# Kernel tuning notes

Measured on AMD Instinct MI355X. Metric: run time of the kernel, lower is better.

Reference implementation:

```python
import jax, jax.numpy as jnp
import numpy as np

TOPK = 3
IOU_THRESHOLD = 0.5


def setup_inputs() -> dict:
    key = jax.random.key(0)
    k0, k1, k2, k3 = jax.random.split(key, 4)
    S, N, TGT_PER_VID = 256, 128, 4
    M = S * TGT_PER_VID          # 1024 target moments total
    P = N * N                    # 16384 valid proposals (mask2d all ones)
    start_offset = jax.random.normal(k0, (S, P), dtype=jnp.float32) * 0.1
    end_offset = jax.random.normal(k1, (S, P), dtype=jnp.float32) * 0.1
    # target moments: (start, end) in [0,1], start <= end
    tgt_moments = jnp.sort(jax.random.uniform(k2, (M, 2), dtype=jnp.float32), axis=1)
    num_targets = jnp.full((S,), TGT_PER_VID, dtype=jnp.int32)  # sums to M
    iou2ds = jax.random.uniform(k3, (M, N, N), dtype=jnp.float32)
    mask2d = jnp.ones((N, N), dtype=bool)
    return {
        "start_offset": start_offset,
        "end_offset": end_offset,
        "tgt_moments": tgt_moments,
        "num_targets": num_targets,
        "iou2ds": iou2ds,
        "mask2d": mask2d,
    }


def reference(start_offset, end_offset, tgt_moments, num_targets, iou2ds, mask2d):
    M, N, _ = iou2ds.shape
    S, P = start_offset.shape
    # map each of the M targets back to its source video (repeat_interleave)
    scatter_m2s = jnp.repeat(jnp.arange(S), num_targets, total_repeat_length=M)
    so = start_offset[scatter_m2s]  # [M, P]
    eo = end_offset[scatter_m2s]    # [M, P]
    # row-major nonzero positions of mask2d (== torch masked_select ordering)
    rows, cols = jnp.nonzero(mask2d, size=P)
    iou1ds = iou2ds[:, rows, cols]  # [M, P]
    # top-k scatter mask + IoU-threshold mask
    _, topk_idx = jax.lax.top_k(iou1ds, TOPK)  # [M, TOPK]
    target_mask = jnp.zeros((M, P), dtype=start_offset.dtype)
    target_mask = target_mask.at[jnp.arange(M)[:, None], topk_idx].set(1.0)
    target_mask = jnp.where(iou1ds > IOU_THRESHOLD, 1.0, target_mask)
    # scores2ds_to_moments: proposal (row, col) -> moment (row/N, (col+1)/N)
    starts = rows.astype(start_offset.dtype) / N                 # [P]
    ends = (cols.astype(start_offset.dtype) + 1.0) / N           # [P]
    start_offset_target = tgt_moments[:, 0:1] - starts[None, :]  # [M, P]
    end_offset_target = tgt_moments[:, 1:2] - ends[None, :]      # [M, P]
    loss = jnp.abs(so - start_offset_target) + jnp.abs(eo - end_offset_target)
    return (loss * target_mask).sum() / target_mask.sum()
```

## Files before the change

kernel.cpp:

```cpp
#include <hip/hip_runtime.h>
#include <math.h>

#define IOU_THR 0.5f
#define NCNT 8
#define FS 8
#define GS 2
#define TPV 4
#define SENT 0x7fffffff

__device__ __forceinline__ bool better(float va, int ia, float vb, int ib) {
    return (va > vb) || (va == vb && ia < ib);
}

__device__ __forceinline__ void merge3(float& a0, float& a1, float& a2,
                                       int& x0, int& x1, int& x2,
                                       float b0, float b1, float b2,
                                       int y0, int y1, int y2) {
    bool t0 = better(a0, x0, b0, y0);
    float ov0 = t0 ? a0 : b0;  int oi0 = t0 ? x0 : y0;
    float ahv = t0 ? a1 : a0;  int ahi = t0 ? x1 : x0;
    float a2v = t0 ? a2 : a1;  int a2i = t0 ? x2 : x1;
    float bhv = t0 ? b0 : b1;  int bhi = t0 ? y0 : y1;
    float b2v = t0 ? b1 : b2;  int b2i = t0 ? y1 : y2;
    bool t1 = better(ahv, ahi, bhv, bhi);
    float ov1 = t1 ? ahv : bhv; int oi1 = t1 ? ahi : bhi;
    float cav = t1 ? a2v : ahv; int cai = t1 ? a2i : ahi;
    float cbv = t1 ? bhv : b2v; int cbi = t1 ? bhi : b2i;
    bool t2 = better(cav, cai, cbv, cbi);
    a0 = ov0; a1 = ov1; a2 = t2 ? cav : cbv;
    x0 = oi0; x1 = oi1; x2 = t2 ? cai : cbi;
}

__global__ void prep_kernel(const int* __restrict__ num_targets,
                            const int* __restrict__ mask2d,
                            int* __restrict__ scatter,
                            int* __restrict__ counts,
                            int* __restrict__ uniform_flag,
                            int S, int M, int P) {
    const int bid = blockIdx.x;
    const int tid = threadIdx.x;

    if (bid < NCNT) {
        const int P4 = P >> 2;
        const int4* __restrict__ m4 = (const int4*)mask2d;
        int c = 0;
        for (int q = bid * 256 + tid; q < P4; q += NCNT * 256) {
            const int4 v = m4[q];
            c += (v.x != 0) + (v.y != 0) + (v.z != 0) + (v.w != 0);
        }
        if (bid == 0) {
            for (int j = (P4 << 2) + tid; j < P; j += 256)
                c += (mask2d[j] != 0);
        }
        __shared__ int red[256];
        red[tid] = c;
        __syncthreads();
        for (int st = 128; st > 0; st >>= 1) {
            if (tid < st) red[tid] += red[tid + st];
            __syncthreads();
        }
        if (tid == 0) counts[bid] = red[0];
    } else {
        __shared__ int cum[1025];
        __shared__ int scn[256];
        __shared__ int uni[256];
        const int chunk = (S + 255) / 256;
        const int sbase = tid * chunk;
        int local[4];
        int csum = 0;
        int ok = 1;
        for (int k = 0; k < chunk && k < 4; ++k) {
            int s = sbase + k;
            int v = (s < S) ? num_targets[s] : TPV;
            if (s < S && v != TPV) ok = 0;
            csum += (s < S) ? v : 0;
            local[k] = csum;
        }
        scn[tid] = csum;
        uni[tid] = ok;
        __syncthreads();
        for (int d = 1; d < 256; d <<= 1) {
            int v = scn[tid];
            int add = (tid >= d) ? scn[tid - d] : 0;
            __syncthreads();
            scn[tid] = v + add;
            __syncthreads();
        }
        for (int st = 128; st > 0; st >>= 1) {
            if (tid < st) uni[tid] &= uni[tid + st];
            __syncthreads();
        }
        {
            int excl = scn[tid] - csum;
            for (int k = 0; k < chunk && k < 4; ++k) {
                int s = sbase + k;
                if (s < S) cum[s + 1] = excl + local[k];
            }
            if (tid == 0) cum[0] = 0;
        }
        __syncthreads();
        const int total = cum[S];
        if (tid == 0)
            uniform_flag[0] = (uni[0] && total == M && M == TPV * S) ? 1 : 0;
        for (int m = tid; m < M; m += 256) {
            int mm = m;
            if (mm >= total) mm = (total > 0) ? (total - 1) : 0;
            int lo = 0, hi = S - 1;
            while (lo < hi) {
                int mid = (lo + hi) >> 1;
                if (cum[mid + 1] <= mm) lo = mid + 1; else hi = mid;
            }
            scatter[m] = lo;
        }
    }
}

__global__ void build_kernel(const int* __restrict__ counts,
                             const int* __restrict__ mask2d,
                             int* __restrict__ rcidx,
                             float* __restrict__ starts,
                             float* __restrict__ ends,
                             int* __restrict__ flag,
                             int N, int P) {
    const int tid = threadIdx.x;
    __shared__ int scan[256];

    scan[tid] = (tid < NCNT) ? counts[tid] : 0;
    __syncthreads();
    for (int st = 128; st > 0; st >>= 1) {
        if (tid < st) scan[tid] += scan[tid + st];
        __syncthreads();
    }
    const int K_all = scan[0];
    const int f = (K_all == P && (P & 3) == 0 && (N & (N - 1)) == 0 && N >= 4) ? 1 : 0;
    if (tid == 0) flag[0] = f;
    if (f) return;
    __syncthreads();

    const int per = (P + 255) / 256;
    const int base = tid * per;
    int cnt = 0;
    for (int k = 0; k < per; ++k) {
        int j = base + k;
        if (j < P && mask2d[j] != 0) cnt++;
    }
    scan[tid] = cnt;
    __syncthreads();
    for (int d = 1; d < 256; d <<= 1) {
        int v = scan[tid];
        int add = (tid >= d) ? scan[tid - d] : 0;
        __syncthreads();
        scan[tid] = v + add;
        __syncthreads();
    }
    const int K = scan[255];
    int pos = scan[tid] - cnt;

    const float fN = (float)N;
    for (int k = 0; k < per; ++k) {
        int j = base + k;
        if (j < P && mask2d[j] != 0) {
            int r = j / N;
            int c = j - r * N;
            rcidx[pos]  = j;
            starts[pos] = (float)r / fN;
            ends[pos]   = (float)(c + 1) / fN;
            pos++;
        }
    }
    __syncthreads();
    for (int j = K + tid; j < P; j += 256) {
        rcidx[j]  = 0;
        starts[j] = 0.0f;
        ends[j]   = 1.0f / fN;
    }
}

__global__ __launch_bounds__(256, 4)
void loss_kernel(const float* __restrict__ start_offset,
                 const float* __restrict__ end_offset,
                 const float* __restrict__ tgt_moments,
                 const int* __restrict__ scatter,
                 const float* __restrict__ iou2ds,
                 const int* __restrict__ rcidx,
                 const float* __restrict__ starts,
                 const float* __restrict__ ends,
                 float* __restrict__ opv, int* __restrict__ opi,
                 double* __restrict__ ops, int* __restrict__ opc,
                 const int* __restrict__ flag,
                 const int* __restrict__ uflag,
                 int P, int M, int N) {
    const int blk = blockIdx.x;
    const int tid = threadIdx.x;
    const int fp  = flag[0];
    const int P4  = P >> 2;
    const bool grouped = fp && uflag[0] && ((M & 1) == 0) &&
                         (P4 % (GS * 256 * 4) == 0);
    const int   lgN  = 31 - __clz(N);
    const float invN = 1.0f / (float)N;

#define PROC(ST, v, jj, so_, eo_, A_, B_)                                   \
    do {                                                                    \
        const bool b0 = (v) > v0##ST;                                       \
        const bool b1 = (v) > v1##ST;                                       \
        const bool b2 = (v) > v2##ST;                                       \
        const float nv0 = fmaxf(v0##ST, (v));                               \
        const float nv1 = __builtin_amdgcn_fmed3f((v), v0##ST, v1##ST);     \
        const float nv2 = __builtin_amdgcn_fmed3f((v), v1##ST, v2##ST);     \
        i2##ST = b1 ? i1##ST : (b2 ? (jj) : i2##ST);                        \
        i1##ST = b0 ? i0##ST : (b1 ? (jj) : i1##ST);                        \
        i0##ST = b0 ? (jj) : i0##ST;                                        \
        v0##ST = nv0; v1##ST = nv1; v2##ST = nv2;                           \
        const bool sel = (v) > IOU_THR;                                     \
        const float l_ = fabsf((so_) - (A_)) + fabsf((eo_) - (B_));         \
        ls##ST += sel ? l_ : 0.0f;                                          \
        lc##ST += sel ? 1 : 0;                                              \
    } while (0)

    if (grouped) {
        if (blk >= M) return;
        int m0, half;
        const int HM = M >> 1;
        if ((HM & 7) == 0 && (M & 3) == 0) {
            const int g = blk % HM, dup = blk / HM;
            m0 = ((g >> 1) << 2) + (dup << 1);
            half = g & 1;
        } else {
            m0 = blk & ~1;
            half = blk & 1;
        }
        const int m1 = m0 + 1;
        const int s  = scatter[m0];

        const float4* __restrict__ so4 = (const float4*)(start_offset + (size_t)s * P);
        const float4* __restrict__ eo4 = (const float4*)(end_offset   + (size_t)s * P);
        const float4* __restrict__ ioA = (const float4*)(iou2ds + (size_t)m0 * P);
        const float4* __restrict__ ioB = (const float4*)(iou2ds + (size_t)m1 * P);
        const float t00 = tgt_moments[2 * m0],     t10 = tgt_moments[2 * m0 + 1];
        const float t01 = tgt_moments[2 * m1],     t11 = tgt_moments[2 * m1 + 1];

        float v0_0 = -INFINITY, v1_0 = -INFINITY, v2_0 = -INFINITY;
        int   i0_0 = SENT, i1_0 = SENT, i2_0 = SENT;
        float ls_0 = 0.f; int lc_0 = 0;
        float v0_1 = -INFINITY, v1_1 = -INFINITY, v2_1 = -INFINITY;
        int   i0_1 = SENT, i1_1 = SENT, i2_1 = SENT;
        float ls_1 = 0.f; int lc_1 = 0;

#define GELEM(q_, VS, VE, VA, VB)                                           \
    do {                                                                    \
        const int j_ = (q_) << 2;                                           \
        const int r_ = j_ >> lgN;                                           \
        const int c_ = j_ & (N - 1);                                        \
        const float stv = (float)r_ * invN;                                 \
        const float en0 = (float)(c_ + 1) * invN;                           \
        const float en1 = en0 + invN;                                       \
        const float en2 = en0 + 2.0f * invN;                                \
        const float en3 = en0 + 3.0f * invN;                                \
        const float A0_ = t00 - stv, A1_ = t01 - stv;                       \
        PROC(_0, (VA).x, j_ + 0, (VS).x, (VE).x, A0_, t10 - en0);           \
        PROC(_0, (VA).y, j_ + 1, (VS).y, (VE).y, A0_, t10 - en1);           \
        PROC(_0, (VA).z, j_ + 2, (VS).z, (VE).z, A0_, t10 - en2);           \
        PROC(_0, (VA).w, j_ + 3, (VS).w, (VE).w, A0_, t10 - en3);           \
        PROC(_1, (VB).x, j_ + 0, (VS).x, (VE).x, A1_, t11 - en0);           \
        PROC(_1, (VB).y, j_ + 1, (VS).y, (VE).y, A1_, t11 - en1);           \
        PROC(_1, (VB).z, j_ + 2, (VS).z, (VE).z, A1_, t11 - en2);           \
        PROC(_1, (VB).w, j_ + 3, (VS).w, (VE).w, A1_, t11 - en3);           \
    } while (0)

        const int qlen  = P4 / GS;
        const int q0    = half * qlen;
        const int iters = qlen >> 8;
        for (int b = 0; b < iters; b += 4) {
            const int qq = q0 + b * 256 + tid;
            const float4 sA = so4[qq],       sB = so4[qq + 256],
                         sC = so4[qq + 512], sD = so4[qq + 768];
            const float4 eA = eo4[qq],       eB = eo4[qq + 256],
                         eC = eo4[qq + 512], eD = eo4[qq + 768];
            const float4 aA = ioA[qq],       aB = ioA[qq + 256],
                         aC = ioA[qq + 512], aD = ioA[qq + 768];
            const float4 bA = ioB[qq],       bB = ioB[qq + 256],
                         bC = ioB[qq + 512], bD = ioB[qq + 768];
            GELEM(qq,       sA, eA, aA, bA);
            GELEM(qq + 256, sB, eB, aB, bB);
            GELEM(qq + 512, sC, eC, aC, bC);
            GELEM(qq + 768, sD, eD, aD, bD);
        }
#undef GELEM

        for (int d = 1; d < 64; d <<= 1) {
            float b0v = __shfl_xor(v0_0, d), b1v = __shfl_xor(v1_0, d), b2v = __shfl_xor(v2_0, d);
            int   y0 = __shfl_xor(i0_0, d), y1 = __shfl_xor(i1_0, d), y2 = __shfl_xor(i2_0, d);
            merge3(v0_0, v1_0, v2_0, i0_0, i1_0, i2_0, b0v, b1v, b2v, y0, y1, y2);
        }
        for (int d = 1; d < 64; d <<= 1) {
            float b0v = __shfl_xor(v0_1, d), b1v = __shfl_xor(v1_1, d), b2v = __shfl_xor(v2_1, d);
            int   y0 = __shfl_xor(i0_1, d), y1 = __shfl_xor(i1_1, d), y2 = __shfl_xor(i2_1, d);
            merge3(v0_1, v1_1, v2_1, i0_1, i1_1, i2_1, b0v, b1v, b2v, y0, y1, y2);
        }
        double ds0 = (double)ls_0, ds1 = (double)ls_1;
        for (int d = 1; d < 64; d <<= 1) {
            ds0 += __shfl_xor(ds0, d); ds1 += __shfl_xor(ds1, d);
            lc_0 += __shfl_xor(lc_0, d); lc_1 += __shfl_xor(lc_1, d);
        }

        __shared__ float  wv[4][2][3];
        __shared__ int    wi[4][2][3];
        __shared__ double wsm[4][2];
        __shared__ int    wct[4][2];
        const int wid  = tid >> 6;
        const int lane = tid & 63;
        if (lane == 0) {
            wv[wid][0][0] = v0_0; wv[wid][0][1] = v1_0; wv[wid][0][2] = v2_0;
            wv[wid][1][0] = v0_1; wv[wid][1][1] = v1_1; wv[wid][1][2] = v2_1;
            wi[wid][0][0] = i0_0; wi[wid][0][1] = i1_0; wi[wid][0][2] = i2_0;
            wi[wid][1][0] = i0_1; wi[wid][1][1] = i1_1; wi[wid][1][2] = i2_1;
            wsm[wid][0] = ds0; wsm[wid][1] = ds1;
            wct[wid][0] = lc_0; wct[wid][1] = lc_1;
        }
        __syncthreads();
        if (tid < 2) {
            const int km = tid;
            float a0 = wv[0][km][0], a1 = wv[0][km][1], a2 = wv[0][km][2];
            int   x0 = wi[0][km][0], x1 = wi[0][km][1], x2 = wi[0][km][2];
            double Sm = wsm[0][km];
            int    Cm = wct[0][km];
            for (int w = 1; w < 4; ++w) {
                merge3(a0, a1, a2, x0, x1, x2,
                       wv[w][km][0], wv[w][km][1], wv[w][km][2],
                       wi[w][km][0], wi[w][km][1], wi[w][km][2]);
                Sm += wsm[w][km];
                Cm += wct[w][km];
            }
            const int slot = (km == 0 ? m0 : m1) * FS + half;
            opv[slot * 3 + 0] = a0; opv[slot * 3 + 1] = a1; opv[slot * 3 + 2] = a2;
            opi[slot * 3 + 0] = x0; opi[slot * 3 + 1] = x1; opi[slot * 3 + 2] = x2;
            ops[slot] = Sm;
            opc[slot] = Cm;
        }
        return;
    }

    const int m  = blk >> 3;
    const int sl = blk & (FS - 1);
    if (m >= M) return;
    const int s = scatter[m];
    const float* __restrict__ so_row  = start_offset + (size_t)s * P;
    const float* __restrict__ eo_row  = end_offset   + (size_t)s * P;
    const float* __restrict__ iou_row = iou2ds       + (size_t)m * P;
    const float tgt0 = tgt_moments[2 * m];
    const float tgt1 = tgt_moments[2 * m + 1];

    float v0_0 = -INFINITY, v1_0 = -INFINITY, v2_0 = -INFINITY;
    int   i0_0 = SENT, i1_0 = SENT, i2_0 = SENT;
    float ls_0 = 0.0f; int lc_0 = 0;

    if (fp) {
        const float4* __restrict__ iou4 = (const float4*)iou_row;
        const float4* __restrict__ so4  = (const float4*)so_row;
        const float4* __restrict__ eo4  = (const float4*)eo_row;
        const int q4len = (P4 + FS - 1) / FS;
        const int q0 = sl * q4len;
        const int qe = min(q0 + q4len, P4);
        for (int q = q0 + tid; q < qe; q += 256) {
            const float4 vi = iou4[q];
            const float4 vs = so4[q];
            const float4 ve = eo4[q];
            const int j_ = q << 2;
            const int r_ = j_ >> lgN;
            const int c_ = j_ & (N - 1);
            const float A_  = tgt0 - (float)r_ * invN;
            const float en0 = (float)(c_ + 1) * invN;
            PROC(_0, vi.x, j_ + 0, vs.x, ve.x, A_, tgt1 - en0);
            PROC(_0, vi.y, j_ + 1, vs.y, ve.y, A_, tgt1 - (en0 + invN));
            PROC(_0, vi.z, j_ + 2, vs.z, ve.z, A_, tgt1 - (en0 + 2.0f * invN));
            PROC(_0, vi.w, j_ + 3, vs.w, ve.w, A_, tgt1 - (en0 + 3.0f * invN));
        }
    } else {
        const int plen = (P + FS - 1) / FS;
        const int j0 = sl * plen;
        const int je = min(j0 + plen, P);
        for (int j = j0 + tid; j < je; j += 256) {
            const int   idx = rcidx[j];
            const float v   = iou_row[idx];
            const float A_  = tgt0 - starts[j];
            const float B_  = tgt1 - ends[j];
            PROC(_0, v, j, so_row[j], eo_row[j], A_, B_);
        }
    }
#undef PROC

    for (int d = 1; d < 64; d <<= 1) {
        float b0v = __shfl_xor(v0_0, d), b1v = __shfl_xor(v1_0, d), b2v = __shfl_xor(v2_0, d);
        int   y0 = __shfl_xor(i0_0, d), y1 = __shfl_xor(i1_0, d), y2 = __shfl_xor(i2_0, d);
        merge3(v0_0, v1_0, v2_0, i0_0, i1_0, i2_0, b0v, b1v, b2v, y0, y1, y2);
    }
    double dsum = (double)ls_0;
    for (int d = 1; d < 64; d <<= 1) dsum += __shfl_xor(dsum, d);
    for (int d = 1; d < 64; d <<= 1) lc_0 += __shfl_xor(lc_0, d);

    __shared__ float  fwv[4][3];
    __shared__ int    fwi[4][3];
    __shared__ double fws[4];
    __shared__ int    fwc[4];
    const int wid  = tid >> 6;
    const int lane = tid & 63;
    if (lane == 0) {
        fwv[wid][0] = v0_0; fwv[wid][1] = v1_0; fwv[wid][2] = v2_0;
        fwi[wid][0] = i0_0; fwi[wid][1] = i1_0; fwi[wid][2] = i2_0;
        fws[wid] = dsum; fwc[wid] = lc_0;
    }
    __syncthreads();
    if (tid == 0) {
        float a0 = fwv[0][0], a1 = fwv[0][1], a2 = fwv[0][2];
        int   x0 = fwi[0][0], x1 = fwi[0][1], x2 = fwi[0][2];
        double Sm = fws[0];
        int    Cm = fwc[0];
        for (int w = 1; w < 4; ++w) {
            merge3(a0, a1, a2, x0, x1, x2,
                   fwv[w][0], fwv[w][1], fwv[w][2],
                   fwi[w][0], fwi[w][1], fwi[w][2]);
            Sm += fws[w];
            Cm += fwc[w];
        }
        const int slot = m * FS + sl;
        opv[slot * 3 + 0] = a0; opv[slot * 3 + 1] = a1; opv[slot * 3 + 2] = a2;
        opi[slot * 3 + 0] = x0; opi[slot * 3 + 1] = x1; opi[slot * 3 + 2] = x2;
        ops[slot] = Sm;
        opc[slot] = Cm;
    }
}

__global__ void merge_finalize_kernel(const float* __restrict__ opv,
                                      const int* __restrict__ opi,
                                      const double* __restrict__ ops,
                                      const int* __restrict__ opc,
                                      const float* __restrict__ start_offset,
                                      const float* __restrict__ end_offset,
                                      const float* __restrict__ tgt_moments,
                                      const int* __restrict__ scatter,
                                      const float* __restrict__ starts,
                                      const float* __restrict__ ends,
                                      const int* __restrict__ flag,
                                      const int* __restrict__ uflag,
                                      float* __restrict__ out,
                                      int P, int M, int N) {
    const int tid = threadIdx.x;
    const int fp  = flag[0];
    const int P4  = P >> 2;
    const bool grouped = fp && uflag[0] && ((M & 1) == 0) &&
                         (P4 % (GS * 256 * 4) == 0);
    const int slices = grouped ? GS : FS;
    const int   lgN  = 31 - __clz(N);
    const float invN = 1.0f / (float)N;

    double S = 0.0;
    int    C = 0;
    for (int m = tid; m < M; m += 1024) {
        const int base = m * FS;
        float a0 = opv[base * 3 + 0], a1 = opv[base * 3 + 1], a2 = opv[base * 3 + 2];
        int   x0 = opi[base * 3 + 0], x1 = opi[base * 3 + 1], x2 = opi[base * 3 + 2];
        double Sm = ops[base];
        int    Cm = opc[base];
        for (int sl = 1; sl < slices; ++sl) {
            const int b = base + sl;
            merge3(a0, a1, a2, x0, x1, x2,
                   opv[b * 3 + 0], opv[b * 3 + 1], opv[b * 3 + 2],
                   opi[b * 3 + 0], opi[b * 3 + 1], opi[b * 3 + 2]);
            Sm += ops[b];
            Cm += opc[b];
        }
        const int s = scatter[m];
        const float* __restrict__ so_row = start_offset + (size_t)s * P;
        const float* __restrict__ eo_row = end_offset   + (size_t)s * P;
        const float tgt0 = tgt_moments[2 * m];
        const float tgt1 = tgt_moments[2 * m + 1];
#define ADDTOP(vk, jk)                                                      \
        do {                                                                \
            if ((jk) != SENT && !((vk) > IOU_THR)) {                        \
                float st_, en_;                                             \
                if (fp) {                                                   \
                    int r_ = (jk) >> lgN, c_ = (jk) & (N - 1);              \
                    st_ = (float)r_ * invN; en_ = (float)(c_ + 1) * invN;   \
                } else { st_ = starts[jk]; en_ = ends[jk]; }                \
                Sm += (double)(fabsf(so_row[jk] - (tgt0 - st_)) +           \
                               fabsf(eo_row[jk] - (tgt1 - en_)));           \
                Cm += 1;                                                    \
            }                                                               \
        } while (0)
        ADDTOP(a0, x0);
        ADDTOP(a1, x1);
        ADDTOP(a2, x2);
#undef ADDTOP
        S += Sm;
        C += Cm;
    }

    for (int d = 1; d < 64; d <<= 1) {
        S += __shfl_xor(S, d);
        C += __shfl_xor(C, d);
    }
    __shared__ double sd[16];
    __shared__ int    sc[16];
    const int wid  = tid >> 6;
    const int lane = tid & 63;
    if (lane == 0) { sd[wid] = S; sc[wid] = C; }
    __syncthreads();
    if (tid == 0) {
        double T = 0.0;
        int    Ct = 0;
        for (int w = 0; w < 16; ++w) { T += sd[w]; Ct += sc[w]; }
        out[0] = (float)(T / (double)Ct);
    }
}

extern "C" void kernel_launch(void* const* d_in, const int* in_sizes, int n_in,
                              void* d_out, int out_size, void* d_ws, size_t ws_size,
                              hipStream_t stream) {
    const float* start_offset = (const float*)d_in[0];
    const float* end_offset   = (const float*)d_in[1];
    const float* tgt_moments  = (const float*)d_in[2];
    const int*   num_targets  = (const int*)d_in[3];
    const float* iou2ds       = (const float*)d_in[4];
    const int*   mask2d       = (const int*)d_in[5];

    const int S = in_sizes[3];
    const int M = in_sizes[2] / 2;
    const int P = in_sizes[0] / S;
    const int NN = in_sizes[5];
    int N = 1;
    while ((long long)N * N < (long long)NN) N++;

    char* ws = (char*)d_ws;
    size_t off = 0;
    const size_t MB = (size_t)M * FS;
    int*    flag    = (int*)(ws + off);    off += 16;
    int*    uflag   = (int*)(ws + off);    off += 16;
    int*    counts  = (int*)(ws + off);    off += (NCNT * 4 + 15) & ~(size_t)15;
    int*    scatter = (int*)(ws + off);    off += ((size_t)M * 4 + 15) & ~(size_t)15;
    int*    rcidx   = (int*)(ws + off);    off += ((size_t)P * 4 + 15) & ~(size_t)15;
    float*  starts  = (float*)(ws + off);  off += ((size_t)P * 4 + 15) & ~(size_t)15;
    float*  ends    = (float*)(ws + off);  off += ((size_t)P * 4 + 15) & ~(size_t)15;
    float*  opv     = (float*)(ws + off);  off += (MB * 12 + 15) & ~(size_t)15;
    int*    opi     = (int*)(ws + off);    off += (MB * 12 + 15) & ~(size_t)15;
    double* ops     = (double*)(ws + off); off += (MB * 8 + 15) & ~(size_t)15;
    int*    opc     = (int*)(ws + off);    off += (MB * 4 + 15) & ~(size_t)15;

    prep_kernel<<<NCNT + 1, 256, 0, stream>>>(num_targets, mask2d, scatter, counts,
                                              uflag, S, M, P);
    build_kernel<<<1, 256, 0, stream>>>(counts, mask2d, rcidx, starts, ends, flag, N, P);
    loss_kernel<<<M * FS, 256, 0, stream>>>(start_offset, end_offset, tgt_moments,
                                            scatter, iou2ds, rcidx, starts, ends,
                                            opv, opi, ops, opc, flag, uflag, P, M, N);
    merge_finalize_kernel<<<1, 1024, 0, stream>>>(opv, opi, ops, opc,
                                                  start_offset, end_offset, tgt_moments,
                                                  scatter, starts, ends, flag, uflag,
                                                  (float*)d_out, P, M, N);
}
```

Measured before the change: 42.61 us.

## Launch exactly M 512-thread blocks and drop manual 4-way load unrolling

The loss kernel used to launch M*8 blocks of 256 threads, of which the grouped path used only M, each handling a pair of targets over half the proposals. It now launches exactly M blocks of 512 threads with a simple strided loop in place of the 4-way unrolled batched float4 loads, and uses a new block-to-work mapping that interleaves groups of 8 blocks. The partial-result layout shrinks to 2 slots per target, so the finalize kernel merges only two partials. The aim is to remove idle launched blocks and reduce per-block partial traffic, at the risk of less memory-level parallelism per thread and a different occupancy balance.

Result: faster. 40.03 us (-6.1%).

```diff
diff --git a/kernel.cpp b/kernel.cpp
--- a/kernel.cpp
+++ b/kernel.cpp
@@ -3,8 +3,8 @@
 
 #define IOU_THR 0.5f
 #define NCNT 8
-#define FS 8
-#define GS 2
+#define THREADS 512
+#define NW (THREADS / 64)
 #define TPV 4
 #define SENT 0x7fffffff
 
@@ -176,7 +176,7 @@
     }
 }
 
-__global__ __launch_bounds__(256, 4)
+__global__ __launch_bounds__(THREADS, 8)
 void loss_kernel(const float* __restrict__ start_offset,
                  const float* __restrict__ end_offset,
                  const float* __restrict__ tgt_moments,
@@ -190,12 +190,13 @@
                  const int* __restrict__ flag,
                  const int* __restrict__ uflag,
                  int P, int M, int N) {
-    const int blk = blockIdx.x;
+    const int bid = blockIdx.x;
     const int tid = threadIdx.x;
     const int fp  = flag[0];
     const int P4  = P >> 2;
+    const int HP4 = P4 >> 1;
     const bool grouped = fp && uflag[0] && ((M & 1) == 0) &&
-                         (P4 % (GS * 256 * 4) == 0);
+                         ((HP4 % THREADS) == 0);
     const int   lgN  = 31 - __clz(N);
     const float invN = 1.0f / (float)N;
 
@@ -218,26 +219,21 @@
     } while (0)
 
     if (grouped) {
-        if (blk >= M) return;
-        int m0, half;
-        const int HM = M >> 1;
-        if ((HM & 7) == 0 && (M & 3) == 0) {
-            const int g = blk % HM, dup = blk / HM;
-            m0 = ((g >> 1) << 2) + (dup << 1);
-            half = g & 1;
-        } else {
-            m0 = blk & ~1;
-            half = blk & 1;
-        }
-        const int m1 = m0 + 1;
-        const int s  = scatter[m0];
+        int idx = bid;
+        if ((M & 7) == 0) idx = (bid & 7) * (M >> 3) + (bid >> 3);
+        const int HM   = M >> 1;
+        const int half = idx / HM;
+        const int pair = idx - half * HM;
+        const int m0   = pair * 2;
+        const int m1   = m0 + 1;
+        const int s    = scatter[m0];
 
         const float4* __restrict__ so4 = (const float4*)(start_offset + (size_t)s * P);
         const float4* __restrict__ eo4 = (const float4*)(end_offset   + (size_t)s * P);
         const float4* __restrict__ ioA = (const float4*)(iou2ds + (size_t)m0 * P);
         const float4* __restrict__ ioB = (const float4*)(iou2ds + (size_t)m1 * P);
-        const float t00 = tgt_moments[2 * m0],     t10 = tgt_moments[2 * m0 + 1];
-        const float t01 = tgt_moments[2 * m1],     t11 = tgt_moments[2 * m1 + 1];
+        const float t00 = tgt_moments[2 * m0], t10 = tgt_moments[2 * m0 + 1];
+        const float t01 = tgt_moments[2 * m1], t11 = tgt_moments[2 * m1 + 1];
 
         float v0_0 = -INFINITY, v1_0 = -INFINITY, v2_0 = -INFINITY;
         int   i0_0 = SENT, i1_0 = SENT, i2_0 = SENT;
@@ -246,46 +242,31 @@
         int   i0_1 = SENT, i1_1 = SENT, i2_1 = SENT;
         float ls_1 = 0.f; int lc_1 = 0;
 
-#define GELEM(q_, VS, VE, VA, VB)                                           \
-    do {                                                                    \
-        const int j_ = (q_) << 2;                                           \
-        const int r_ = j_ >> lgN;                                           \
-        const int c_ = j_ & (N - 1);                                        \
-        const float stv = (float)r_ * invN;                                 \
-        const float en0 = (float)(c_ + 1) * invN;                           \
-        const float en1 = en0 + invN;                                       \
-        const float en2 = en0 + 2.0f * invN;                                \
-        const float en3 = en0 + 3.0f * invN;                                \
-        const float A0_ = t00 - stv, A1_ = t01 - stv;                       \
-        PROC(_0, (VA).x, j_ + 0, (VS).x, (VE).x, A0_, t10 - en0);           \
-        PROC(_0, (VA).y, j_ + 1, (VS).y, (VE).y, A0_, t10 - en1);           \
-        PROC(_0, (VA).z, j_ + 2, (VS).z, (VE).z, A0_, t10 - en2);           \
-        PROC(_0, (VA).w, j_ + 3, (VS).w, (VE).w, A0_, t10 - en3);           \
-        PROC(_1, (VB).x, j_ + 0, (VS).x, (VE).x, A1_, t11 - en0);           \
-        PROC(_1, (VB).y, j_ + 1, (VS).y, (VE).y, A1_, t11 - en1);           \
-        PROC(_1, (VB).z, j_ + 2, (VS).z, (VE).z, A1_, t11 - en2);           \
-        PROC(_1, (VB).w, j_ + 3, (VS).w, (VE).w, A1_, t11 - en3);           \
-    } while (0)
-
-        const int qlen  = P4 / GS;
-        const int q0    = half * qlen;
-        const int iters = qlen >> 8;
-        for (int b = 0; b < iters; b += 4) {
-            const int qq = q0 + b * 256 + tid;
-            const float4 sA = so4[qq],       sB = so4[qq + 256],
-                         sC = so4[qq + 512], sD = so4[qq + 768];
-            const float4 eA = eo4[qq],       eB = eo4[qq + 256],
-                         eC = eo4[qq + 512], eD = eo4[qq + 768];
-            const float4 aA = ioA[qq],       aB = ioA[qq + 256],
-                         aC = ioA[qq + 512], aD = ioA[qq + 768];
-            const float4 bA = ioB[qq],       bB = ioB[qq + 256],
-                         bC = ioB[qq + 512], bD = ioB[qq + 768];
-            GELEM(qq,       sA, eA, aA, bA);
-            GELEM(qq + 256, sB, eB, aB, bB);
-            GELEM(qq + 512, sC, eC, aC, bC);
-            GELEM(qq + 768, sD, eD, aD, bD);
-        }
-#undef GELEM
+        const int q0 = half * HP4;
+        const int qe = q0 + HP4;
+        for (int q = q0 + tid; q < qe; q += THREADS) {
+            const float4 vs = so4[q];
+            const float4 ve = eo4[q];
+            const float4 va = ioA[q];
+            const float4 vb = ioB[q];
+            const int j_ = q << 2;
+            const int r_ = j_ >> lgN;
+            const int c_ = j_ & (N - 1);
+            const float stv = (float)r_ * invN;
+            const float en0 = (float)(c_ + 1) * invN;
+            const float en1 = en0 + invN;
+            const float en2 = en0 + 2.0f * invN;
+            const float en3 = en0 + 3.0f * invN;
+            const float A0_ = t00 - stv, A1_ = t01 - stv;
+            PROC(_0, va.x, j_ + 0, vs.x, ve.x, A0_, t10 - en0);
+            PROC(_0, va.y, j_ + 1, vs.y, ve.y, A0_, t10 - en1);
+            PROC(_0, va.z, j_ + 2, vs.z, ve.z, A0_, t10 - en2);
+            PROC(_0, va.w, j_ + 3, vs.w, ve.w, A0_, t10 - en3);
+            PROC(_1, vb.x, j_ + 0, vs.x, ve.x, A1_, t11 - en0);
+            PROC(_1, vb.y, j_ + 1, vs.y, ve.y, A1_, t11 - en1);
+            PROC(_1, vb.z, j_ + 2, vs.z, ve.z, A1_, t11 - en2);
+            PROC(_1, vb.w, j_ + 3, vs.w, ve.w, A1_, t11 - en3);
+        }
 
         for (int d = 1; d < 64; d <<= 1) {
             float b0v = __shfl_xor(v0_0, d), b1v = __shfl_xor(v1_0, d), b2v = __shfl_xor(v2_0, d);
@@ -303,17 +284,17 @@
             lc_0 += __shfl_xor(lc_0, d); lc_1 += __shfl_xor(lc_1, d);
         }
 
-        __shared__ float  wv[4][2][3];
-        __shared__ int    wi[4][2][3];
-        __shared__ double wsm[4][2];
-        __shared__ int    wct[4][2];
+        __shared__ float  wv[NW][2][3];
+        __shared__ int    wix[NW][2][3];
+        __shared__ double wsm[NW][2];
+        __shared__ int    wct[NW][2];
         const int wid  = tid >> 6;
         const int lane = tid & 63;
         if (lane == 0) {
             wv[wid][0][0] = v0_0; wv[wid][0][1] = v1_0; wv[wid][0][2] = v2_0;
             wv[wid][1][0] = v0_1; wv[wid][1][1] = v1_1; wv[wid][1][2] = v2_1;
-            wi[wid][0][0] = i0_0; wi[wid][0][1] = i1_0; wi[wid][0][2] = i2_0;
-            wi[wid][1][0] = i0_1; wi[wid][1][1] = i1_1; wi[wid][1][2] = i2_1;
+            wix[wid][0][0] = i0_0; wix[wid][0][1] = i1_0; wix[wid][0][2] = i2_0;
+            wix[wid][1][0] = i0_1; wix[wid][1][1] = i1_1; wix[wid][1][2] = i2_1;
             wsm[wid][0] = ds0; wsm[wid][1] = ds1;
             wct[wid][0] = lc_0; wct[wid][1] = lc_1;
         }
@@ -321,17 +302,17 @@
         if (tid < 2) {
             const int km = tid;
             float a0 = wv[0][km][0], a1 = wv[0][km][1], a2 = wv[0][km][2];
-            int   x0 = wi[0][km][0], x1 = wi[0][km][1], x2 = wi[0][km][2];
+            int   x0 = wix[0][km][0], x1 = wix[0][km][1], x2 = wix[0][km][2];
             double Sm = wsm[0][km];
             int    Cm = wct[0][km];
-            for (int w = 1; w < 4; ++w) {
+            for (int w = 1; w < NW; ++w) {
                 merge3(a0, a1, a2, x0, x1, x2,
                        wv[w][km][0], wv[w][km][1], wv[w][km][2],
-                       wi[w][km][0], wi[w][km][1], wi[w][km][2]);
+                       wix[w][km][0], wix[w][km][1], wix[w][km][2]);
                 Sm += wsm[w][km];
                 Cm += wct[w][km];
             }
-            const int slot = (km == 0 ? m0 : m1) * FS + half;
+            const int slot = ((km == 0 ? m0 : m1) << 1) + half;
             opv[slot * 3 + 0] = a0; opv[slot * 3 + 1] = a1; opv[slot * 3 + 2] = a2;
             opi[slot * 3 + 0] = x0; opi[slot * 3 + 1] = x1; opi[slot * 3 + 2] = x2;
             ops[slot] = Sm;
@@ -340,8 +321,7 @@
         return;
     }
 
-    const int m  = blk >> 3;
-    const int sl = blk & (FS - 1);
+    const int m = bid;
     if (m >= M) return;
     const int s = scatter[m];
     const float* __restrict__ so_row  = start_offset + (size_t)s * P;
@@ -358,10 +338,7 @@
         const float4* __restrict__ iou4 = (const float4*)iou_row;
         const float4* __restrict__ so4  = (const float4*)so_row;
         const float4* __restrict__ eo4  = (const float4*)eo_row;
-        const int q4len = (P4 + FS - 1) / FS;
-        const int q0 = sl * q4len;
-        const int qe = min(q0 + q4len, P4);
-        for (int q = q0 + tid; q < qe; q += 256) {
+        for (int q = tid; q < P4; q += THREADS) {
             const float4 vi = iou4[q];
             const float4 vs = so4[q];
             const float4 ve = eo4[q];
@@ -376,10 +353,7 @@
             PROC(_0, vi.w, j_ + 3, vs.w, ve.w, A_, tgt1 - (en0 + 3.0f * invN));
         }
     } else {
-        const int plen = (P + FS - 1) / FS;
-        const int j0 = sl * plen;
-        const int je = min(j0 + plen, P);
-        for (int j = j0 + tid; j < je; j += 256) {
+        for (int j = tid; j < P; j += THREADS) {
             const int   idx = rcidx[j];
             const float v   = iou_row[idx];
             const float A_  = tgt0 - starts[j];
@@ -398,10 +372,10 @@
     for (int d = 1; d < 64; d <<= 1) dsum += __shfl_xor(dsum, d);
     for (int d = 1; d < 64; d <<= 1) lc_0 += __shfl_xor(lc_0, d);
 
-    __shared__ float  fwv[4][3];
-    __shared__ int    fwi[4][3];
-    __shared__ double fws[4];
-    __shared__ int    fwc[4];
+    __shared__ float  fwv[NW][3];
+    __shared__ int    fwi[NW][3];
+    __shared__ double fws[NW];
+    __shared__ int    fwc[NW];
     const int wid  = tid >> 6;
     const int lane = tid & 63;
     if (lane == 0) {
@@ -415,18 +389,26 @@
         int   x0 = fwi[0][0], x1 = fwi[0][1], x2 = fwi[0][2];
         double Sm = fws[0];
         int    Cm = fwc[0];
-        for (int w = 1; w < 4; ++w) {
+        for (int w = 1; w < NW; ++w) {
             merge3(a0, a1, a2, x0, x1, x2,
                    fwv[w][0], fwv[w][1], fwv[w][2],
                    fwi[w][0], fwi[w][1], fwi[w][2]);
             Sm += fws[w];
             Cm += fwc[w];
         }
-        const int slot = m * FS + sl;
+        const int slot = m << 1;
         opv[slot * 3 + 0] = a0; opv[slot * 3 + 1] = a1; opv[slot * 3 + 2] = a2;
         opi[slot * 3 + 0] = x0; opi[slot * 3 + 1] = x1; opi[slot * 3 + 2] = x2;
         ops[slot] = Sm;
         opc[slot] = Cm;
+        opv[(slot + 1) * 3 + 0] = -INFINITY;
+        opv[(slot + 1) * 3 + 1] = -INFINITY;
+        opv[(slot + 1) * 3 + 2] = -INFINITY;
+        opi[(slot + 1) * 3 + 0] = SENT;
+        opi[(slot + 1) * 3 + 1] = SENT;
+        opi[(slot + 1) * 3 + 2] = SENT;
+        ops[slot + 1] = 0.0;
+        opc[slot + 1] = 0;
     }
 }
 
@@ -441,34 +423,25 @@
                                       const float* __restrict__ starts,
                                       const float* __restrict__ ends,
                                       const int* __restrict__ flag,
-                                      const int* __restrict__ uflag,
                                       float* __restrict__ out,
                                       int P, int M, int N) {
     const int tid = threadIdx.x;
     const int fp  = flag[0];
-    const int P4  = P >> 2;
-    const bool grouped = fp && uflag[0] && ((M & 1) == 0) &&
-                         (P4 % (GS * 256 * 4) == 0);
-    const int slices = grouped ? GS : FS;
     const int   lgN  = 31 - __clz(N);
     const float invN = 1.0f / (float)N;
 
     double S = 0.0;
-    int    C = 0;
+    long long C = 0;
     for (int m = tid; m < M; m += 1024) {
-        const int base = m * FS;
-        float a0 = opv[base * 3 + 0], a1 = opv[base * 3 + 1], a2 = opv[base * 3 + 2];
-        int   x0 = opi[base * 3 + 0], x1 = opi[base * 3 + 1], x2 = opi[base * 3 + 2];
-        double Sm = ops[base];
-        int    Cm = opc[base];
-        for (int sl = 1; sl < slices; ++sl) {
-            const int b = base + sl;
-            merge3(a0, a1, a2, x0, x1, x2,
-                   opv[b * 3 + 0], opv[b * 3 + 1], opv[b * 3 + 2],
-                   opi[b * 3 + 0], opi[b * 3 + 1], opi[b * 3 + 2]);
-            Sm += ops[b];
-            Cm += opc[b];
-        }
+        const int b0 = (m << 1), b1 = b0 + 1;
+        float a0 = opv[b0 * 3 + 0], a1 = opv[b0 * 3 + 1], a2 = opv[b0 * 3 + 2];
+        int   x0 = opi[b0 * 3 + 0], x1 = opi[b0 * 3 + 1], x2 = opi[b0 * 3 + 2];
+        merge3(a0, a1, a2, x0, x1, x2,
+               opv[b1 * 3 + 0], opv[b1 * 3 + 1], opv[b1 * 3 + 2],
+               opi[b1 * 3 + 0], opi[b1 * 3 + 1], opi[b1 * 3 + 2]);
+        double Sm = ops[b0] + ops[b1];
+        int    Cm = opc[b0] + opc[b1];
+
         const int s = scatter[m];
         const float* __restrict__ so_row = start_offset + (size_t)s * P;
         const float* __restrict__ eo_row = end_offset   + (size_t)s * P;
@@ -500,14 +473,14 @@
         C += __shfl_xor(C, d);
     }
     __shared__ double sd[16];
-    __shared__ int    sc[16];
+    __shared__ long long sc[16];
     const int wid  = tid >> 6;
     const int lane = tid & 63;
     if (lane == 0) { sd[wid] = S; sc[wid] = C; }
     __syncthreads();
     if (tid == 0) {
         double T = 0.0;
-        int    Ct = 0;
+        long long Ct = 0;
         for (int w = 0; w < 16; ++w) { T += sd[w]; Ct += sc[w]; }
         out[0] = (float)(T / (double)Ct);
     }
@@ -532,7 +505,7 @@
 
     char* ws = (char*)d_ws;
     size_t off = 0;
-    const size_t MB = (size_t)M * FS;
+    const size_t SLOTS = (size_t)M * 2;
     int*    flag    = (int*)(ws + off);    off += 16;
     int*    uflag   = (int*)(ws + off);    off += 16;
     int*    counts  = (int*)(ws + off);    off += (NCNT * 4 + 15) & ~(size_t)15;
@@ -540,19 +513,19 @@
     int*    rcidx   = (int*)(ws + off);    off += ((size_t)P * 4 + 15) & ~(size_t)15;
     float*  starts  = (float*)(ws + off);  off += ((size_t)P * 4 + 15) & ~(size_t)15;
     float*  ends    = (float*)(ws + off);  off += ((size_t)P * 4 + 15) & ~(size_t)15;
-    float*  opv     = (float*)(ws + off);  off += (MB * 12 + 15) & ~(size_t)15;
-    int*    opi     = (int*)(ws + off);    off += (MB * 12 + 15) & ~(size_t)15;
-    double* ops     = (double*)(ws + off); off += (MB * 8 + 15) & ~(size_t)15;
-    int*    opc     = (int*)(ws + off);    off += (MB * 4 + 15) & ~(size_t)15;
+    float*  opv     = (float*)(ws + off);  off += (SLOTS * 12 + 15) & ~(size_t)15;
+    int*    opi     = (int*)(ws + off);    off += (SLOTS * 12 + 15) & ~(size_t)15;
+    double* ops     = (double*)(ws + off); off += (SLOTS * 8 + 15) & ~(size_t)15;
+    int*    opc     = (int*)(ws + off);    off += (SLOTS * 4 + 15) & ~(size_t)15;
 
     prep_kernel<<<NCNT + 1, 256, 0, stream>>>(num_targets, mask2d, scatter, counts,
                                               uflag, S, M, P);
     build_kernel<<<1, 256, 0, stream>>>(counts, mask2d, rcidx, starts, ends, flag, N, P);
-    loss_kernel<<<M * FS, 256, 0, stream>>>(start_offset, end_offset, tgt_moments,
-                                            scatter, iou2ds, rcidx, starts, ends,
-                                            opv, opi, ops, opc, flag, uflag, P, M, N);
+    loss_kernel<<<M, THREADS, 0, stream>>>(start_offset, end_offset, tgt_moments,
+                                           scatter, iou2ds, rcidx, starts, ends,
+                                           opv, opi, ops, opc, flag, uflag, P, M, N);
     merge_finalize_kernel<<<1, 1024, 0, stream>>>(opv, opi, ops, opc,
                                                   start_offset, end_offset, tgt_moments,
-                                                  scatter, starts, ends, flag, uflag,
+                                                  scatter, starts, ends, flag,
                                                   (float*)d_out, P, M, N);
 }
```
